# Performance work log

Measured on AMD Instinct MI355X. Metric: run time of the kernel, lower is better.

The kernel has to match this reference:

```python
import jax, jax.numpy as jnp
import numpy as np
from math import sqrt

B, T, C = 2, 2048, 2048
H = 16
NOPE, ROPE, VD, LORA = 128, 64, 128, 512
QK = NOPE + ROPE  # 192
EPS = 1e-6


def _make_freq_cis(T, rope_dim):
    inv = 1.0 / (10000.0 ** (np.arange(0, rope_dim, 2, dtype=np.float32) / rope_dim))
    t = np.arange(T, dtype=np.float32)
    ang = np.outer(t, inv)  # [T, rope_dim/2]
    return jnp.asarray(np.stack([np.cos(ang), np.sin(ang)], -1))  # [T, rope_dim/2, 2]


def setup_inputs() -> dict:
    key = jax.random.key(0)
    ks = jax.random.split(key, 6)
    x = jax.random.normal(ks[0], (B, T, C), jnp.float32)
    freq_cis = _make_freq_cis(T, ROPE)
    causal = jnp.where(jnp.tril(jnp.ones((T, T), bool)), 0.0, -1e9).astype(jnp.float32)
    Wq = jax.random.normal(ks[1], (C, H * QK), jnp.float32) * (1.0 / sqrt(C))
    Wckv = jax.random.normal(ks[2], (C, LORA + ROPE), jnp.float32) * (1.0 / sqrt(C))
    kv_norm_w = jnp.ones((LORA,), jnp.float32)
    Wdkv = jax.random.normal(ks[3], (LORA, H * (NOPE + VD)), jnp.float32) * (1.0 / sqrt(LORA))
    Wproj = jax.random.normal(ks[4], (H * VD, C), jnp.float32) * (1.0 / sqrt(H * VD))
    return {"x": x, "freq_cis": freq_cis, "mask": causal, "window": causal,
            "Wq": Wq, "Wckv": Wckv, "kv_norm_w": kv_norm_w, "Wdkv": Wdkv,
            "Wproj": Wproj, "start_pos": 0}


def apply_rope(x, freq_cis):
    # x: [B, T, h, D]; freq_cis: [T, D/2, 2]
    b, t, h, d = x.shape
    xr = x.reshape(b, t, h, d // 2, 2)
    fc = freq_cis.reshape(1, t, 1, d // 2, 2)
    real = xr[..., 0] * fc[..., 0] - xr[..., 1] * fc[..., 1]
    imag = xr[..., 1] * fc[..., 0] + xr[..., 0] * fc[..., 1]
    return jnp.stack([real, imag], -1).reshape(b, t, h, d)


def rms_norm(x, w, eps=EPS):
    return x * jax.lax.rsqrt(jnp.mean(x * x, -1, keepdims=True) + eps) * w


def reference(x, freq_cis, mask, window, Wq, Wckv, kv_norm_w, Wdkv, Wproj, start_pos):
    del window, start_pos  # Global attention, no KV cache (prefill)
    b, t, _ = x.shape
    q = (x @ Wq).reshape(b, t, H, QK)
    q_nope, q_rope = q[..., :NOPE], q[..., NOPE:]
    q_rope = apply_rope(q_rope, freq_cis)

    ckv = x @ Wckv  # [B, T, LORA+ROPE]
    kv_lat, k_rope = ckv[..., :LORA], ckv[..., LORA:]
    k_rope = apply_rope(k_rope.reshape(b, t, 1, ROPE), freq_cis)  # [B,T,1,ROPE]

    kv = rms_norm(kv_lat, kv_norm_w) @ Wdkv  # [B, T, H*(NOPE+VD)]
    kv = kv.reshape(b, t, H, NOPE + VD)
    k_nope, v = kv[..., :NOPE], kv[..., NOPE:]

    q = jnp.concatenate([q_nope, q_rope], -1)                                   # [B,T,H,QK]
    k = jnp.concatenate([k_nope, jnp.broadcast_to(k_rope, (b, t, H, ROPE))], -1)

    scale = 1.0 / sqrt(QK)
    atten = jnp.einsum('bqhd,bkhd->bhqk', q, k) * scale + mask  # [B,H,T,T]
    atten = jax.nn.softmax(atten, -1)
    out = jnp.einsum('bhqk,bkhd->bqhd', atten, v).reshape(b, t, H * VD)
    return out @ Wproj
```

## Files before the change

### kernel.cpp

```cpp
#include <hip/hip_runtime.h>
#include <hip/hip_bf16.h>
#include <math.h>


typedef short bf16x8 __attribute__((ext_vector_type(8)));
typedef short short4v __attribute__((ext_vector_type(4)));
typedef float f32x4 __attribute__((ext_vector_type(4)));
typedef float f32x16 __attribute__((ext_vector_type(16)));

#define MFMA16(a, b, c) __builtin_amdgcn_mfma_f32_16x16x32_bf16(a, b, c, 0, 0, 0)
#define MFMA32(a, b, c) __builtin_amdgcn_mfma_f32_32x32x16_bf16(a, b, c, 0, 0, 0)

__device__ __forceinline__ short f2bf(float f) {
  union { float f; unsigned u; } v; v.f = f;
  unsigned r = v.u + 0x7fffu + ((v.u >> 16) & 1u);
  return (short)(r >> 16);
}
__device__ __forceinline__ float bf2f(short s) {
  union { unsigned u; float f; } v;
  v.u = ((unsigned)(unsigned short)s) << 16;
  return v.f;
}
__device__ __forceinline__ unsigned cvtpk(float a, float b) {
  unsigned r;
  asm("v_cvt_pk_bf16_f32 %0, %1, %2" : "=v"(r) : "v"(a), "v"(b));
  return r;
}
__device__ __forceinline__ void gl16(const void* g, void* l) {
  __builtin_amdgcn_global_load_lds(
      (const __attribute__((address_space(1))) unsigned int*)g,
      (__attribute__((address_space(3))) unsigned int*)l, 16, 0, 0);
}
#define CFENCE() asm volatile("" ::: "memory")
#define HWBAR()  do { CFENCE(); __builtin_amdgcn_s_barrier(); CFENCE(); } while (0)

__global__ __launch_bounds__(256) void cvt_k(const float* __restrict__ in,
                                             short* __restrict__ out, int n) {
  int i = (blockIdx.x * 256 + threadIdx.x) * 8;
  if (i >= n) return;
  float4 a = *(const float4*)(in + i);
  float4 b = *(const float4*)(in + i + 4);
  bf16x8 o;
  o[0] = f2bf(a.x); o[1] = f2bf(a.y); o[2] = f2bf(a.z); o[3] = f2bf(a.w);
  o[4] = f2bf(b.x); o[5] = f2bf(b.y); o[6] = f2bf(b.z); o[7] = f2bf(b.w);
  *(bf16x8*)(out + i) = o;
}

__global__ __launch_bounds__(256) void tcvt_k(const float* __restrict__ W,
                                              short* __restrict__ out,
                                              int K, int N, int Np, int row_off) {
  __shared__ float tile[32][33];
  int k0 = blockIdx.x * 32, n0 = blockIdx.y * 32;
  int tx = threadIdx.x & 31, ty = threadIdx.x >> 5;
#pragma unroll
  for (int j = 0; j < 4; j++) {
    int k = k0 + ty + j * 8, n = n0 + tx;
    tile[ty + j * 8][tx] = (n < N) ? W[(size_t)k * N + n] : 0.f;
  }
  __syncthreads();
#pragma unroll
  for (int j = 0; j < 4; j++) {
    int n = n0 + ty + j * 8;
    out[(size_t)(row_off + n) * K + k0 + tx] = f2bf(tile[tx][ty + j * 8]);
  }
}

template <int MODE, int BM, int BN, int SGL>
__global__ __launch_bounds__(512, 2) void gemm8_k(const short* __restrict__ A,
                                                  const short* __restrict__ Bt,
                                                  void* __restrict__ C1,
                                                  void* __restrict__ C2,
                                                  int M, int N, int K, int nbx) {
  constexpr int FM = BM / 32;
  constexpr int FN = BN / 64;
  constexpr int XCH = (BM * 4) / 512;
  constexpr int YCH = (BN * 4) / 512;
  __shared__ short lX[3][BM * 32];
  __shared__ short lY[3][BN * 32];

  const int nwg = gridDim.x;
  const int cpx = nwg >> 3;
  const int swz = (blockIdx.x & 7) * cpx + (blockIdx.x >> 3);
  const int bx = swz % nbx, by = swz / nbx;
  const int m0 = bx * BM, n0 = by * BN;
  const int tid = threadIdx.x, lane = tid & 63, wave = tid >> 6;
  const int wm = wave >> 2, wn = wave & 3;
  const int l15 = lane & 15, l4 = lane >> 4;
  const int nt = K >> 5;

  auto stage = [&](int t) {
    int kk = t << 5;
    short* bX = &lX[t % 3][0];
    short* bY = &lY[t % 3][0];
#pragma unroll
    for (int c = 0; c < XCH; c++) {
      int idx = c * 512 + tid;
      int row = idx >> 2, seg = idx & 3;
      gl16(A + (size_t)(m0 + row) * K + kk + ((seg ^ ((row >> 1) & 3)) << 3),
           bX + idx * 8);
    }
#pragma unroll
    for (int c = 0; c < YCH; c++) {
      int idx = c * 512 + tid;
      int row = idx >> 2, seg = idx & 3;
      gl16(Bt + (size_t)(n0 + row) * K + kk + ((seg ^ ((row >> 1) & 3)) << 3),
           bY + idx * 8);
    }
  };

  f32x4 zero = {0.f, 0.f, 0.f, 0.f};
  f32x4 acc[FM][FN];
#pragma unroll
  for (int i = 0; i < FM; i++)
#pragma unroll
    for (int j = 0; j < FN; j++) acc[i][j] = zero;

  stage(0);
  stage(1);
  if constexpr (SGL == 4) asm volatile("s_waitcnt vmcnt(4)" ::: "memory");
  else                    asm volatile("s_waitcnt vmcnt(3)" ::: "memory");
  HWBAR();

  for (int t = 0; t < nt; t++) {
    const short* bX = &lX[t % 3][0];
    const short* bY = &lY[t % 3][0];
    bf16x8 xf[FM / 2], yf[FN];
#pragma unroll
    for (int i = 0; i < FM / 2; i++) {
      int row = wm * (BM / 2) + i * 16 + l15;
      xf[i] = *(const bf16x8*)&bX[row * 32 + ((l4 ^ ((row >> 1) & 3)) << 3)];
    }
#pragma unroll
    for (int j = 0; j < FN; j++) {
      int row = wn * (BN / 4) + j * 16 + l15;
      yf[j] = *(const bf16x8*)&bY[row * 32 + ((l4 ^ ((row >> 1) & 3)) << 3)];
    }
    bool st = (t + 2 < nt);
    if (st) stage(t + 2);
    HWBAR();
    __builtin_amdgcn_sched_barrier(0);
    __builtin_amdgcn_s_setprio(1);
#pragma unroll
    for (int i = 0; i < FM / 2; i++)
#pragma unroll
      for (int j = 0; j < FN; j++) acc[i][j] = MFMA16(xf[i], yf[j], acc[i][j]);
    __builtin_amdgcn_s_setprio(0);
    bf16x8 xg[FM / 2];
#pragma unroll
    for (int i = 0; i < FM / 2; i++) {
      int row = wm * (BM / 2) + (FM / 2 + i) * 16 + l15;
      xg[i] = *(const bf16x8*)&bX[row * 32 + ((l4 ^ ((row >> 1) & 3)) << 3)];
    }
    if (st) {
      if constexpr (SGL == 4) asm volatile("s_waitcnt vmcnt(4) lgkmcnt(0)" ::: "memory");
      else                    asm volatile("s_waitcnt vmcnt(3) lgkmcnt(0)" ::: "memory");
    } else {
      asm volatile("s_waitcnt vmcnt(0) lgkmcnt(0)" ::: "memory");
    }
    HWBAR();
    __builtin_amdgcn_sched_barrier(0);
    __builtin_amdgcn_s_setprio(1);
#pragma unroll
    for (int i = 0; i < FM / 2; i++)
#pragma unroll
      for (int j = 0; j < FN; j++)
        acc[FM / 2 + i][j] = MFMA16(xg[i], yf[j], acc[FM / 2 + i][j]);
    __builtin_amdgcn_s_setprio(0);
  }

#pragma unroll
  for (int i = 0; i < FM; i++) {
#pragma unroll
    for (int j = 0; j < FN; j++) {
      int m_ = m0 + wm * (BM / 2) + i * 16 + l4 * 4;
      int n = n0 + wn * (BN / 4) + j * 16 + l15;
      if (n >= N) continue;
      if (MODE == 2) {
        int bb = m_ >> 11, t2 = m_ & 2047, hh = n >> 8, c = n & 255;
        if (c < 128) {
#pragma unroll
          for (int r = 0; r < 4; r++)
            ((short*)C1)[((size_t)(bb * 16 + hh) * 2048 + t2 + r) * 192 + c] =
                f2bf(acc[i][j][r]);
        } else {
          short4v pk;
#pragma unroll
          for (int r = 0; r < 4; r++) pk[r] = f2bf(acc[i][j][r]);
          *(short4v*)&((short*)C2)[((size_t)(bb * 16 + hh) * 128 + (c - 128)) * 2048 + t2] = pk;
        }
      } else {
#pragma unroll
        for (int r = 0; r < 4; r++) {
          float v = acc[i][j][r];
          if (MODE == 0)
            ((short*)C1)[(size_t)(m_ + r) * N + n] = f2bf(v);
          else
            ((float*)C1)[(size_t)(m_ + r) * N + n] = v;
        }
      }
    }
  }
}

__global__ __launch_bounds__(256) void rmsnorm_k(const short* __restrict__ qc,
                                                 const float* __restrict__ w,
                                                 short* __restrict__ out) {
  int row = blockIdx.x * 4 + (threadIdx.x >> 6);
  int lane = threadIdx.x & 63;
  const short* src = qc + (size_t)row * 3712 + 3072 + lane * 8;
  bf16x8 v = *(const bf16x8*)src;
  float f[8];
  float ss = 0.f;
#pragma unroll
  for (int j = 0; j < 8; j++) { f[j] = bf2f(v[j]); ss += f[j] * f[j]; }
#pragma unroll
  for (int m = 1; m < 64; m <<= 1) ss += __shfl_xor(ss, m);
  float r = rsqrtf(ss * (1.f / 512.f) + 1e-6f);
  bf16x8 o;
#pragma unroll
  for (int j = 0; j < 8; j++) o[j] = f2bf(f[j] * r * w[lane * 8 + j]);
  *(bf16x8*)(out + (size_t)row * 512 + lane * 8) = o;
}

__global__ __launch_bounds__(256) void qrope_k(const short* __restrict__ qc,
                                               const float* __restrict__ freq,
                                               short* __restrict__ q_all) {
  int g = blockIdx.x * 256 + threadIdx.x;
  int row = g / 24, part = g % 24;
  int b = row >> 15, h = (row >> 11) & 15, t = row & 2047;
  const short* src = qc + (size_t)(b * 2048 + t) * 3712 + h * 192;
  short* dst = q_all + (size_t)row * 192;
  const float scale = 0.10411756f;
  if (part < 16) {
    bf16x8 v = *(const bf16x8*)(src + part * 8);
    bf16x8 o;
#pragma unroll
    for (int j = 0; j < 8; j++) o[j] = f2bf(bf2f(v[j]) * scale);
    *(bf16x8*)(dst + part * 8) = o;
  } else {
    int q = part - 16;
    bf16x8 v = *(const bf16x8*)(src + 128 + q * 8);
    float4 fa = *(const float4*)(freq + t * 64 + q * 8);
    float4 fb = *(const float4*)(freq + t * 64 + q * 8 + 4);
    float cs[8] = {fa.x, fa.y, fa.z, fa.w, fb.x, fb.y, fb.z, fb.w};
    bf16x8 o;
#pragma unroll
    for (int j = 0; j < 4; j++) {
      float c = cs[2 * j], s = cs[2 * j + 1];
      float x0 = bf2f(v[2 * j]), x1 = bf2f(v[2 * j + 1]);
      o[2 * j] = f2bf((x0 * c - x1 * s) * scale);
      o[2 * j + 1] = f2bf((x1 * c + x0 * s) * scale);
    }
    *(bf16x8*)(dst + 128 + q * 8) = o;
  }
}

__global__ __launch_bounds__(64) void krope_k(const short* __restrict__ qc,
                                              const float* __restrict__ freq,
                                              short* __restrict__ k_all) {
  int bt = blockIdx.x;
  int lane = threadIdx.x;
  int b = bt >> 11, t = bt & 2047;
  const short* src = qc + (size_t)bt * 3712 + 3584;
  int p = lane >> 1;
  float c = freq[t * 64 + p * 2], s = freq[t * 64 + p * 2 + 1];
  float x0 = bf2f(src[2 * p]), x1 = bf2f(src[2 * p + 1]);
  float v = (lane & 1) ? (x1 * c + x0 * s) : (x0 * c - x1 * s);
  short vb = f2bf(v);
#pragma unroll
  for (int h = 0; h < 16; h++)
    k_all[((size_t)(b * 16 + h) * 2048 + t) * 192 + 128 + lane] = vb;
}

__device__ __forceinline__ void stage6(const short* __restrict__ Kp,
                                       const short* __restrict__ VT,
                                       short* kb, short* vb, int kt, int ptid) {
#pragma unroll
  for (int c = 0; c < 6; c++) {
    int idx = c * 256 + ptid;
    if (idx < 832) {
      int r = idx / 25; if (r > 31) r = 31;
      int s = idx % 25;
      int s2 = (s >= 24) ? 0 : s;
      gl16(Kp + (size_t)(kt + r) * 192 + s2 * 8, kb + idx * 8);
    } else {
      int v = idx - 832;
      int r = v / 5; if (r > 127) r = 127;
      int s = v % 5;
      int s2 = (s >= 4) ? 0 : s;
      gl16(VT + (size_t)r * 2048 + kt + s2 * 8, vb + v * 8);
    }
  }
}

__global__ __launch_bounds__(512, 2) void attn_k(const short* __restrict__ q_all,
                                                 const short* __restrict__ k_all,
                                                 const short* __restrict__ vt,
                                                 short* __restrict__ attn_out) {
  __shared__ short kbuf[3][832 * 8];
  __shared__ short vbuf[3][704 * 8];
  int bh = blockIdx.x;
  int b = bh >> 4, h = bh & 15;
  int col = gridDim.y - 1 - blockIdx.y;
  int tid = threadIdx.x;
  int wave = tid >> 6, lane = tid & 63;
  int l31 = lane & 31, hi = lane >> 5;
  const bool producer = (wave >= 4);
  int qw = col * 128 + (wave & 3) * 32;
  int qrow = qw + l31;
  const short* Q = q_all + ((size_t)bh * 2048 + qrow) * 192;
  const short* Kp = k_all + (size_t)bh * 2048 * 192;
  const short* VT = vt + (size_t)bh * 128 * 2048;
  int sig = (l31 & 19) | ((l31 >> 1) & 4) | ((l31 << 1) & 8);

  bf16x8 qf[12];
  f32x16 o[4];
  f32x16 sInit, zro;
#pragma unroll
  for (int r = 0; r < 16; r++) { sInit[r] = -28.8539f; zro[r] = 0.f; }
  float lsum = 0.f;
  if (!producer) {
#pragma unroll
    for (int kb = 0; kb < 12; kb++)
      qf[kb] = *(const bf16x8*)(Q + kb * 16 + hi * 8);
#pragma unroll
    for (int vb = 0; vb < 4; vb++)
#pragma unroll
      for (int r = 0; r < 16; r++) o[vb][r] = 0.f;
  }

  const int nt = (col * 128 + 128) >> 5;

  if (producer) {
    stage6(Kp, VT, kbuf[0], vbuf[0], 0, tid - 256);
    if (nt > 1) stage6(Kp, VT, kbuf[1], vbuf[1], 32, tid - 256);
    asm volatile("s_waitcnt vmcnt(6)" ::: "memory");
  }
  HWBAR();

  for (int t = 0; t < nt; t++) {
    if (producer) {
      if (t + 2 < nt) {
        stage6(Kp, VT, kbuf[(t + 2) % 3], vbuf[(t + 2) % 3], (t + 2) << 5, tid - 256);
        asm volatile("s_waitcnt vmcnt(6)" ::: "memory");
      } else {
        asm volatile("s_waitcnt vmcnt(0)" ::: "memory");
      }
    } else {
      int kt = t << 5;
      int cur = t % 3;
      if (kt < qw + 32) {
        f32x16 sc = sInit, sc2 = zro;
        __builtin_amdgcn_s_setprio(1);
#pragma unroll
        for (int kb = 0; kb < 6; kb++) {
          int c0 = 2 * kb + hi, c1 = 2 * (kb + 6) + hi;
          bf16x8 kf0 = *(const bf16x8*)&kbuf[cur][sig * 200 + (c0 << 3)];
          bf16x8 kf1 = *(const bf16x8*)&kbuf[cur][sig * 200 + (c1 << 3)];
          sc = MFMA32(kf0, qf[kb], sc);
          sc2 = MFMA32(kf1, qf[kb + 6], sc2);
        }
        __builtin_amdgcn_s_setprio(0);
#pragma unroll
        for (int r = 0; r < 16; r++) sc[r] += sc2[r];
        unsigned pw[8];
        if (kt + 32 <= qw) {
#pragma unroll
          for (int r2 = 0; r2 < 8; r2++) {
            float pa = exp2f(sc[2 * r2]);
            float pb = exp2f(sc[2 * r2 + 1]);
            lsum += pa + pb;
            pw[r2] = cvtpk(pa, pb);
          }
        } else {
#pragma unroll
          for (int r2 = 0; r2 < 8; r2++) {
            int r = 2 * r2;
            int key = kt + (r & 3) + 4 * ((r >> 2) & 1) + 8 * hi + 16 * (r >> 3);
            float va = (key <= qrow) ? sc[r] : -1e30f;
            float vb2 = (key + 1 <= qrow) ? sc[r + 1] : -1e30f;
            float pa = exp2f(va);
            float pb = exp2f(vb2);
            lsum += pa + pb;
            pw[r2] = cvtpk(pa, pb);
          }
        }
        union { unsigned u[4]; bf16x8 v; } p0, p1;
#pragma unroll
        for (int w = 0; w < 4; w++) { p0.u[w] = pw[w]; p1.u[w] = pw[4 + w]; }
        __builtin_amdgcn_s_setprio(1);
#pragma unroll
        for (int vb = 0; vb < 4; vb++) {
          int vcol = vb * 32 + l31;
          bf16x8 vf0 = *(const bf16x8*)&vbuf[cur][vcol * 40 + (hi << 3)];
          bf16x8 vf1 = *(const bf16x8*)&vbuf[cur][vcol * 40 + ((2 + hi) << 3)];
          o[vb] = MFMA32(vf0, p0.v, o[vb]);
          o[vb] = MFMA32(vf1, p1.v, o[vb]);
        }
        __builtin_amdgcn_s_setprio(0);
      }
    }
    HWBAR();
  }

  if (!producer) {
    lsum += __shfl_xor(lsum, 32);
    float inv = 1.f / lsum;
    size_t base = ((size_t)b * 2048 + qrow) * 2048 + h * 128;
#pragma unroll
    for (int vb = 0; vb < 4; vb++) {
#pragma unroll
      for (int r2 = 0; r2 < 8; r2++) {
        int r = 2 * r2;
        int v = vb * 32 + (r & 3) + 8 * (r >> 2) + 4 * hi;
        unsigned pk2 = ((unsigned)(unsigned short)f2bf(o[vb][r] * inv)) |
                       (((unsigned)(unsigned short)f2bf(o[vb][r + 1] * inv)) << 16);
        *(unsigned*)(attn_out + base + v) = pk2;
      }
    }
  }
}

extern "C" void kernel_launch(void* const* d_in, const int* in_sizes, int n_in,
                              void* d_out, int out_size, void* d_ws, size_t ws_size,
                              hipStream_t stream) {
  const float* x = (const float*)d_in[0];
  const float* freq = (const float*)d_in[1];
  const float* Wq = (const float*)d_in[4];
  const float* Wckv = (const float*)d_in[5];
  const float* kvw = (const float*)d_in[6];
  const float* Wdkv = (const float*)d_in[7];
  const float* Wproj = (const float*)d_in[8];

  char* ws = (char*)d_ws;
  size_t off = 0;
  auto alloc = [&](size_t bytes) {
    size_t o = off;
    off += (bytes + 255) & ~(size_t)255;
    return o;
  };
  size_t o_xbf = alloc(4096ull * 2048 * 2);
  size_t o_wqc = alloc(3840ull * 2048 * 2);
  size_t o_wdkv = alloc(4096ull * 512 * 2);
  size_t o_wproj = alloc(2048ull * 2048 * 2);
  size_t o_qc = alloc(4096ull * 3712 * 2);
  size_t o_kvlat = alloc(4096ull * 512 * 2);
  size_t o_qall = alloc(32ull * 2048 * 192 * 2);
  size_t o_kall = alloc(32ull * 2048 * 192 * 2);
  size_t o_vt = alloc(32ull * 128 * 2048 * 2);
  size_t o_attn = o_xbf;

  short* x_bf = (short*)(ws + o_xbf);
  short* wqc = (short*)(ws + o_wqc);
  short* wdkv = (short*)(ws + o_wdkv);
  short* wproj = (short*)(ws + o_wproj);
  short* qc = (short*)(ws + o_qc);
  short* kvlat = (short*)(ws + o_kvlat);
  short* qall = (short*)(ws + o_qall);
  short* kall = (short*)(ws + o_kall);
  short* vtb = (short*)(ws + o_vt);
  short* attnb = (short*)(ws + o_attn);

  cvt_k<<<4096, 256, 0, stream>>>(x, x_bf, 4096 * 2048);
  tcvt_k<<<dim3(64, 96), 256, 0, stream>>>(Wq, wqc, 2048, 3072, 3072, 0);
  tcvt_k<<<dim3(64, 24), 256, 0, stream>>>(Wckv, wqc, 2048, 576, 768, 3072);
  tcvt_k<<<dim3(16, 128), 256, 0, stream>>>(Wdkv, wdkv, 512, 4096, 4096, 0);
  tcvt_k<<<dim3(64, 64), 256, 0, stream>>>(Wproj, wproj, 2048, 2048, 2048, 0);

  gemm8_k<0, 256, 256, 4><<<240, 512, 0, stream>>>(x_bf, wqc, qc, nullptr,
                                                   4096, 3712, 2048, 16);

  rmsnorm_k<<<1024, 256, 0, stream>>>(qc, kvw, kvlat);
  qrope_k<<<6144, 256, 0, stream>>>(qc, freq, qall);
  krope_k<<<4096, 64, 0, stream>>>(qc, freq, kall);

  gemm8_k<2, 256, 256, 4><<<256, 512, 0, stream>>>(kvlat, wdkv, kall, vtb,
                                                   4096, 4096, 512, 16);

  attn_k<<<dim3(32, 16), 512, 0, stream>>>(qall, kall, vtb, attnb);

  gemm8_k<1, 128, 256, 3><<<256, 512, 0, stream>>>(attnb, wproj, d_out, nullptr,
                                                   4096, 2048, 2048, 32);
}
```

Measured before the change: 275.0 us.

## Scatter Q/KV projection epilogue directly and merge weight conversion kernels

The first projection GEMM now writes q_nope (pre-scaled) straight into the per-head Q buffer, and writes the rope slices and the KV latent into separate compact buffers. This replaces the intermediate 3712-wide qc buffer and lets the rope kernels handle only the 64-wide rope parts. The four weight transpose-convert launches are also merged into one kernel that dispatches on block index. In exchange, the GEMM epilogue does scattered 2-byte stores with div/mod by 192, which may be less coalesced than the old row-major writes.

```diff
diff --git a/kernel.cpp b/kernel.cpp
--- a/kernel.cpp
+++ b/kernel.cpp
@@ -46,11 +46,21 @@
   *(bf16x8*)(out + i) = o;
 }
 
-__global__ __launch_bounds__(256) void tcvt_k(const float* __restrict__ W,
-                                              short* __restrict__ out,
-                                              int K, int N, int Np, int row_off) {
+__global__ __launch_bounds__(256) void wcvt_k(const float* __restrict__ Wq,
+                                              const float* __restrict__ Wckv,
+                                              const float* __restrict__ Wdkv,
+                                              const float* __restrict__ Wproj,
+                                              short* __restrict__ wqc,
+                                              short* __restrict__ wdkv,
+                                              short* __restrict__ wproj) {
   __shared__ float tile[32][33];
-  int k0 = blockIdx.x * 32, n0 = blockIdx.y * 32;
+  int id = blockIdx.x;
+  const float* W; short* out; int K, N, gx, row_off, idx;
+  if (id < 6144)      { idx = id;        W = Wq;    out = wqc;   K = 2048; N = 3072; gx = 64; row_off = 0; }
+  else if (id < 7680) { idx = id - 6144; W = Wckv;  out = wqc;   K = 2048; N = 576;  gx = 64; row_off = 3072; }
+  else if (id < 9728) { idx = id - 7680; W = Wdkv;  out = wdkv;  K = 512;  N = 4096; gx = 16; row_off = 0; }
+  else                { idx = id - 9728; W = Wproj; out = wproj; K = 2048; N = 2048; gx = 64; row_off = 0; }
+  int k0 = (idx % gx) * 32, n0 = (idx / gx) * 32;
   int tx = threadIdx.x & 31, ty = threadIdx.x >> 5;
 #pragma unroll
   for (int j = 0; j < 4; j++) {
@@ -70,6 +80,8 @@
                                                   const short* __restrict__ Bt,
                                                   void* __restrict__ C1,
                                                   void* __restrict__ C2,
+                                                  void* __restrict__ C3,
+                                                  void* __restrict__ C4,
                                                   int M, int N, int K, int nbx) {
   constexpr int FM = BM / 32;
   constexpr int FN = BN / 64;
@@ -188,6 +200,30 @@
           for (int r = 0; r < 4; r++) pk[r] = f2bf(acc[i][j][r]);
           *(short4v*)&((short*)C2)[((size_t)(bb * 16 + hh) * 128 + (c - 128)) * 2048 + t2] = pk;
         }
+      } else if (MODE == 3) {
+        int bb = m_ >> 11, t2 = m_ & 2047;
+        if (n < 3072) {
+          int hh = n / 192, c = n % 192;
+          size_t rowb = (size_t)(bb * 16 + hh) * 2048 + t2;
+          if (c < 128) {
+#pragma unroll
+            for (int r = 0; r < 4; r++)
+              ((short*)C1)[(rowb + r) * 192 + c] = f2bf(acc[i][j][r] * 0.10411756f);
+          } else {
+#pragma unroll
+            for (int r = 0; r < 4; r++)
+              ((short*)C2)[(rowb + r) * 64 + (c - 128)] = f2bf(acc[i][j][r]);
+          }
+        } else if (n < 3584) {
+          int c2 = n - 3072;
+#pragma unroll
+          for (int r = 0; r < 4; r++)
+            ((short*)C3)[(size_t)(bb * 2048 + t2 + r) * 512 + c2] = f2bf(acc[i][j][r]);
+        } else if (n < 3648) {
+#pragma unroll
+          for (int r = 0; r < 4; r++)
+            ((short*)C4)[(size_t)(bb * 2048 + t2 + r) * 64 + (n - 3584)] = f2bf(acc[i][j][r]);
+        }
       } else {
 #pragma unroll
         for (int r = 0; r < 4; r++) {
@@ -202,12 +238,12 @@
   }
 }
 
-__global__ __launch_bounds__(256) void rmsnorm_k(const short* __restrict__ qc,
+__global__ __launch_bounds__(256) void rmsnorm_k(const short* __restrict__ kvraw,
                                                  const float* __restrict__ w,
                                                  short* __restrict__ out) {
   int row = blockIdx.x * 4 + (threadIdx.x >> 6);
   int lane = threadIdx.x & 63;
-  const short* src = qc + (size_t)row * 3712 + 3072 + lane * 8;
+  const short* src = kvraw + (size_t)row * 512 + lane * 8;
   bf16x8 v = *(const bf16x8*)src;
   float f[8];
   float ss = 0.f;
@@ -222,49 +258,38 @@
   *(bf16x8*)(out + (size_t)row * 512 + lane * 8) = o;
 }
 
-__global__ __launch_bounds__(256) void qrope_k(const short* __restrict__ qc,
+__global__ __launch_bounds__(256) void qrope2_k(const short* __restrict__ qrs,
+                                                const float* __restrict__ freq,
+                                                short* __restrict__ q_all) {
+  int g = blockIdx.x * 256 + threadIdx.x;
+  int row = g >> 3, p = g & 7;
+  int t = row & 2047;
+  const float scale = 0.10411756f;
+  bf16x8 v = *(const bf16x8*)(qrs + (size_t)row * 64 + p * 8);
+  float4 fa = *(const float4*)(freq + t * 64 + p * 8);
+  float4 fb = *(const float4*)(freq + t * 64 + p * 8 + 4);
+  float cs[8] = {fa.x, fa.y, fa.z, fa.w, fb.x, fb.y, fb.z, fb.w};
+  bf16x8 o;
+#pragma unroll
+  for (int j = 0; j < 4; j++) {
+    float c = cs[2 * j], s = cs[2 * j + 1];
+    float x0 = bf2f(v[2 * j]), x1 = bf2f(v[2 * j + 1]);
+    o[2 * j] = f2bf((x0 * c - x1 * s) * scale);
+    o[2 * j + 1] = f2bf((x1 * c + x0 * s) * scale);
+  }
+  *(bf16x8*)(q_all + (size_t)row * 192 + 128 + p * 8) = o;
+}
+
+__global__ __launch_bounds__(64) void krope2_k(const short* __restrict__ krs,
                                                const float* __restrict__ freq,
-                                               short* __restrict__ q_all) {
-  int g = blockIdx.x * 256 + threadIdx.x;
-  int row = g / 24, part = g % 24;
-  int b = row >> 15, h = (row >> 11) & 15, t = row & 2047;
-  const short* src = qc + (size_t)(b * 2048 + t) * 3712 + h * 192;
-  short* dst = q_all + (size_t)row * 192;
-  const float scale = 0.10411756f;
-  if (part < 16) {
-    bf16x8 v = *(const bf16x8*)(src + part * 8);
-    bf16x8 o;
-#pragma unroll
-    for (int j = 0; j < 8; j++) o[j] = f2bf(bf2f(v[j]) * scale);
-    *(bf16x8*)(dst + part * 8) = o;
-  } else {
-    int q = part - 16;
-    bf16x8 v = *(const bf16x8*)(src + 128 + q * 8);
-    float4 fa = *(const float4*)(freq + t * 64 + q * 8);
-    float4 fb = *(const float4*)(freq + t * 64 + q * 8 + 4);
-    float cs[8] = {fa.x, fa.y, fa.z, fa.w, fb.x, fb.y, fb.z, fb.w};
-    bf16x8 o;
-#pragma unroll
-    for (int j = 0; j < 4; j++) {
-      float c = cs[2 * j], s = cs[2 * j + 1];
-      float x0 = bf2f(v[2 * j]), x1 = bf2f(v[2 * j + 1]);
-      o[2 * j] = f2bf((x0 * c - x1 * s) * scale);
-      o[2 * j + 1] = f2bf((x1 * c + x0 * s) * scale);
-    }
-    *(bf16x8*)(dst + 128 + q * 8) = o;
-  }
-}
-
-__global__ __launch_bounds__(64) void krope_k(const short* __restrict__ qc,
-                                              const float* __restrict__ freq,
-                                              short* __restrict__ k_all) {
+                                               short* __restrict__ k_all) {
   int bt = blockIdx.x;
   int lane = threadIdx.x;
   int b = bt >> 11, t = bt & 2047;
-  const short* src = qc + (size_t)bt * 3712 + 3584;
   int p = lane >> 1;
   float c = freq[t * 64 + p * 2], s = freq[t * 64 + p * 2 + 1];
-  float x0 = bf2f(src[2 * p]), x1 = bf2f(src[2 * p + 1]);
+  float x0 = bf2f(krs[(size_t)bt * 64 + 2 * p]);
+  float x1 = bf2f(krs[(size_t)bt * 64 + 2 * p + 1]);
   float v = (lane & 1) ? (x1 * c + x0 * s) : (x0 * c - x1 * s);
   short vb = f2bf(v);
 #pragma unroll
@@ -443,7 +468,9 @@
   size_t o_wqc = alloc(3840ull * 2048 * 2);
   size_t o_wdkv = alloc(4096ull * 512 * 2);
   size_t o_wproj = alloc(2048ull * 2048 * 2);
-  size_t o_qc = alloc(4096ull * 3712 * 2);
+  size_t o_qrs = alloc(32ull * 2048 * 64 * 2);
+  size_t o_kvraw = alloc(4096ull * 512 * 2);
+  size_t o_krs = alloc(4096ull * 64 * 2);
   size_t o_kvlat = alloc(4096ull * 512 * 2);
   size_t o_qall = alloc(32ull * 2048 * 192 * 2);
   size_t o_kall = alloc(32ull * 2048 * 192 * 2);
@@ -454,7 +481,9 @@
   short* wqc = (short*)(ws + o_wqc);
   short* wdkv = (short*)(ws + o_wdkv);
   short* wproj = (short*)(ws + o_wproj);
-  short* qc = (short*)(ws + o_qc);
+  short* qrs = (short*)(ws + o_qrs);
+  short* kvraw = (short*)(ws + o_kvraw);
+  short* krs = (short*)(ws + o_krs);
   short* kvlat = (short*)(ws + o_kvlat);
   short* qall = (short*)(ws + o_qall);
   short* kall = (short*)(ws + o_kall);
@@ -462,23 +491,20 @@
   short* attnb = (short*)(ws + o_attn);
 
   cvt_k<<<4096, 256, 0, stream>>>(x, x_bf, 4096 * 2048);
-  tcvt_k<<<dim3(64, 96), 256, 0, stream>>>(Wq, wqc, 2048, 3072, 3072, 0);
-  tcvt_k<<<dim3(64, 24), 256, 0, stream>>>(Wckv, wqc, 2048, 576, 768, 3072);
-  tcvt_k<<<dim3(16, 128), 256, 0, stream>>>(Wdkv, wdkv, 512, 4096, 4096, 0);
-  tcvt_k<<<dim3(64, 64), 256, 0, stream>>>(Wproj, wproj, 2048, 2048, 2048, 0);
-
-  gemm8_k<0, 256, 256, 4><<<240, 512, 0, stream>>>(x_bf, wqc, qc, nullptr,
+  wcvt_k<<<13824, 256, 0, stream>>>(Wq, Wckv, Wdkv, Wproj, wqc, wdkv, wproj);
+
+  gemm8_k<3, 256, 256, 4><<<240, 512, 0, stream>>>(x_bf, wqc, qall, qrs, kvraw, krs,
                                                    4096, 3712, 2048, 16);
 
-  rmsnorm_k<<<1024, 256, 0, stream>>>(qc, kvw, kvlat);
-  qrope_k<<<6144, 256, 0, stream>>>(qc, freq, qall);
-  krope_k<<<4096, 64, 0, stream>>>(qc, freq, kall);
-
-  gemm8_k<2, 256, 256, 4><<<256, 512, 0, stream>>>(kvlat, wdkv, kall, vtb,
+  rmsnorm_k<<<1024, 256, 0, stream>>>(kvraw, kvw, kvlat);
+  qrope2_k<<<2048, 256, 0, stream>>>(qrs, freq, qall);
+  krope2_k<<<4096, 64, 0, stream>>>(krs, freq, kall);
+
+  gemm8_k<2, 256, 256, 4><<<256, 512, 0, stream>>>(kvlat, wdkv, kall, vtb, nullptr, nullptr,
                                                    4096, 4096, 512, 16);
 
   attn_k<<<dim3(32, 16), 512, 0, stream>>>(qall, kall, vtb, attnb);
 
-  gemm8_k<1, 128, 256, 3><<<256, 512, 0, stream>>>(attnb, wproj, d_out, nullptr,
+  gemm8_k<1, 128, 256, 3><<<256, 512, 0, stream>>>(attnb, wproj, d_out, nullptr, nullptr, nullptr,
                                                    4096, 2048, 2048, 32);
 }
```

Result: faster. 263.3 us (-4.3%).
